# Optimization experiments

Hardware: AMD Instinct MI355X
Metric: run time of the kernel (lower is better)

The kernel has to match this reference:

```python
import jax, jax.numpy as jnp
import numpy as np
from jax.ops import segment_sum

N, E, F, H, G, T = 50000, 800000, 128, 256, 512, 4


def setup_inputs() -> dict:
    key = jax.random.key(0)
    ks = jax.random.split(key, 12)
    x = jax.random.normal(ks[0], (N, F), jnp.float32)
    edge_index = jax.random.randint(ks[1], (2, E), 0, N)
    batch = jnp.sort(jax.random.randint(ks[2], (N,), 0, G))
    num_atoms = jax.random.normal(ks[3], (G, 1), jnp.float32)
    def lin(k, fan_in, fan_out):
        s = 1.0 / np.sqrt(fan_in)
        return jax.random.uniform(k, (fan_in, fan_out), jnp.float32, -s, s)
    W1 = lin(ks[4], F, H); b1 = jnp.zeros((H,), jnp.float32)
    W2 = lin(ks[5], H, H); b2 = jnp.zeros((H,), jnp.float32)
    W3 = lin(ks[6], H + 1, 32); b3 = jnp.zeros((32,), jnp.float32)
    W4 = lin(ks[7], 32, T); b4 = jnp.zeros((T,), jnp.float32)
    return {"x": x, "edge_index": edge_index, "batch": batch, "num_atoms": num_atoms,
            "W1": W1, "b1": b1, "W2": W2, "b2": b2, "W3": W3, "b3": b3, "W4": W4, "b4": b4}


def _gcn_norm(edge_index, num_nodes):
    # PyG GCNConv default: add self-loops, symmetric D^-1/2 A D^-1/2 normalization
    loop = jnp.arange(num_nodes, dtype=edge_index.dtype)
    src = jnp.concatenate([edge_index[0], loop])
    dst = jnp.concatenate([edge_index[1], loop])
    deg = segment_sum(jnp.ones_like(dst, jnp.float32), dst, num_segments=num_nodes)
    dinv = jnp.where(deg > 0, jax.lax.rsqrt(jnp.maximum(deg, 1e-12)), 0.0)
    norm = dinv[src] * dinv[dst]  # [E+N]
    return src, dst, norm


def _gcn_conv(x, W, b, src, dst, norm, num_nodes):
    h = x @ W  # [N, out]
    agg = segment_sum(h[src] * norm[:, None], dst, num_segments=num_nodes)
    return agg + b


def reference(x, edge_index, batch, num_atoms, W1, b1, W2, b2, W3, b3, W4, b4):
    n = x.shape[0]
    src, dst, norm = _gcn_norm(edge_index, n)
    h = jax.nn.relu(_gcn_conv(x, W1, b1, src, dst, norm, n))   # dropout = identity (eval)
    h = jax.nn.relu(_gcn_conv(h, W2, b2, src, dst, norm, n))
    # global mean pool over graphs
    sums = segment_sum(h, batch, num_segments=G)               # [G, H]
    cnt = segment_sum(jnp.ones((n,), jnp.float32), batch, num_segments=G)
    pooled = sums / jnp.maximum(cnt, 1.0)[:, None]
    z = jnp.concatenate([pooled, num_atoms], axis=1)           # [G, H+1]
    z = jax.nn.relu(z @ W3 + b3)
    return z @ W4 + b4                                         # [G, T]
```

## Files before the change

### kernel.cpp

```cpp
#include <hip/hip_runtime.h>
#include <hip/hip_bf16.h>
#include <hip/hip_fp8.h>


#define NN 50000
#define EE 800000
#define FDIM 128
#define HDIM 256
#define GG 512
#define SCAN_NB ((NN + 255) / 256)

typedef __attribute__((ext_vector_type(8))) short short8;
typedef __attribute__((ext_vector_type(4))) float floatx4;
typedef __attribute__((ext_vector_type(2))) float floatx2;

__device__ __forceinline__ unsigned short f2bf(float f) {
    unsigned u = __float_as_uint(f);
    return (unsigned short)((u + 0x7FFF + ((u >> 16) & 1)) >> 16);
}
__device__ __forceinline__ float bflo(unsigned v) { return __uint_as_float(v << 16); }
__device__ __forceinline__ float bfhi(unsigned v) { return __uint_as_float(v & 0xFFFF0000u); }

__device__ __forceinline__ unsigned char enc8(float v) {
#if defined(__has_builtin) && __has_builtin(__builtin_amdgcn_cvt_pk_fp8_f32)
    return (unsigned char)(__builtin_amdgcn_cvt_pk_fp8_f32(v, v, 0, false) & 0xFF);
#else
    __hip_fp8_e4m3 q(v);
    return (unsigned char)q.__x;
#endif
}
__device__ __forceinline__ void dec4(int d, float* f) {
#if defined(__has_builtin) && __has_builtin(__builtin_amdgcn_cvt_pk_f32_fp8)
    floatx2 lo = __builtin_amdgcn_cvt_pk_f32_fp8(d, false);
    floatx2 hi = __builtin_amdgcn_cvt_pk_f32_fp8(d, true);
    f[0] = lo.x; f[1] = lo.y; f[2] = hi.x; f[3] = hi.y;
#else
    unsigned u = (unsigned)d;
    #pragma unroll
    for (int i = 0; i < 4; ++i) {
        __hip_fp8_e4m3 t; t.__x = (__hip_fp8_storage_t)((u >> (8 * i)) & 0xFF);
        f[i] = (float)t;
    }
#endif
}

__device__ __forceinline__ void gload16(const void* g, void* l) {
    __builtin_amdgcn_global_load_lds((const __attribute__((address_space(1))) void*)g,
                                     (__attribute__((address_space(3))) void*)l, 16, 0, 0);
}


__global__ void hist_kernel(const int* __restrict__ dst, int* __restrict__ deg,
                            int* __restrict__ epos, int e) {
    int i = blockIdx.x * blockDim.x + threadIdx.x;
    int stride = gridDim.x * blockDim.x;
    for (; i < e; i += stride) epos[i] = atomicAdd(&deg[dst[i]], 1);
}

__global__ __launch_bounds__(256) void scan_part(const int* __restrict__ deg,
                                                 int* __restrict__ row_off,
                                                 int* __restrict__ blk_sums,
                                                 float* __restrict__ dinv, int n) {
    __shared__ int s[256];
    int tid = threadIdx.x;
    int i = blockIdx.x * 256 + tid;
    int v = (i < n) ? deg[i] : 0;
    if (i < n) dinv[i] = rsqrtf((float)v + 1.0f);
    s[tid] = v;
    __syncthreads();
    #pragma unroll
    for (int off = 1; off < 256; off <<= 1) {
        int t = (tid >= off) ? s[tid - off] : 0;
        __syncthreads();
        s[tid] += t;
        __syncthreads();
    }
    if (i < n) row_off[i] = s[tid] - v;
    if (tid == 255) blk_sums[blockIdx.x] = s[255];
}

__global__ __launch_bounds__(256) void scan_sums(int* __restrict__ blk_sums, int nb) {
    __shared__ int s[256];
    int tid = threadIdx.x;
    int v = (tid < nb) ? blk_sums[tid] : 0;
    s[tid] = v;
    __syncthreads();
    #pragma unroll
    for (int off = 1; off < 256; off <<= 1) {
        int t = (tid >= off) ? s[tid - off] : 0;
        __syncthreads();
        s[tid] += t;
        __syncthreads();
    }
    if (tid < nb) blk_sums[tid] = s[tid] - v;
}

__global__ __launch_bounds__(256) void scan_add(int* __restrict__ row_off,
                                                const int* __restrict__ blk_sums,
                                                int n, int e) {
    int i = blockIdx.x * 256 + threadIdx.x;
    if (i < n) row_off[i] += blk_sums[blockIdx.x];
    if (i == 0) row_off[n] = e;
}

__global__ void scatter_kernel(const int* __restrict__ src, const int* __restrict__ dst,
                               const int* __restrict__ row_off, const int* __restrict__ epos,
                               const float* __restrict__ dinv,
                               int2* __restrict__ csr, int e) {
    int i = blockIdx.x * blockDim.x + threadIdx.x;
    int stride = gridDim.x * blockDim.x;
    for (; i < e; i += stride) {
        int s = src[i], d = dst[i];
        int pos = row_off[d] + epos[i];
        csr[pos] = make_int2(s, __float_as_int(dinv[s] * dinv[d]));
    }
}

#define XCHUNKS (NN * FDIM / 4)
#define CAST_TOTAL (XCHUNKS + FDIM * HDIM + HDIM * HDIM + NN / 4 + GG * HDIM / 4)
__global__ __launch_bounds__(256) void cast_all(const float* __restrict__ x,
                                                unsigned short* __restrict__ x_bf,
                                                const float* __restrict__ W1,
                                                unsigned short* __restrict__ W1t,
                                                const float* __restrict__ W2,
                                                unsigned short* __restrict__ W2t,
                                                int* __restrict__ deg,
                                                float* __restrict__ pool) {
    int idx = blockIdx.x * 256 + threadIdx.x;
    if (idx < XCHUNKS) {
        int i = idx * 4;
        float4 v = *(const float4*)&x[i];
        ushort4 o;
        o.x = f2bf(v.x); o.y = f2bf(v.y); o.z = f2bf(v.z); o.w = f2bf(v.w);
        *(ushort4*)&x_bf[i] = o;
        return;
    }
    int r = idx - XCHUNKS;
    if (r < FDIM * HDIM) {
        int nn = r / FDIM, k = r - nn * FDIM;
        W1t[r] = f2bf(W1[(size_t)k * HDIM + nn]);
        return;
    }
    r -= FDIM * HDIM;
    if (r < HDIM * HDIM) {
        int nn = r / HDIM, k = r - nn * HDIM;
        W2t[r] = f2bf(W2[(size_t)k * HDIM + nn]);
        return;
    }
    r -= HDIM * HDIM;
    if (r < NN / 4) {
        int4 z = {0, 0, 0, 0};
        *(int4*)&deg[r * 4] = z;
        return;
    }
    r -= NN / 4;
    if (r < GG * HDIM / 4) {
        float4 z = {0.f, 0.f, 0.f, 0.f};
        *(float4*)&pool[r * 4] = z;
    }
}


#define FMA8(v, wgt) do { unsigned _u; \
    _u = (unsigned)(v).x; acc0 = fmaf(bflo(_u), (wgt), acc0); acc1 = fmaf(bfhi(_u), (wgt), acc1); \
    _u = (unsigned)(v).y; acc2 = fmaf(bflo(_u), (wgt), acc2); acc3 = fmaf(bfhi(_u), (wgt), acc3); \
    _u = (unsigned)(v).z; acc4 = fmaf(bflo(_u), (wgt), acc4); acc5 = fmaf(bfhi(_u), (wgt), acc5); \
    _u = (unsigned)(v).w; acc6 = fmaf(bflo(_u), (wgt), acc6); acc7 = fmaf(bfhi(_u), (wgt), acc7); } while (0)

__device__ __forceinline__ void fma16(const int4& g, float wgt, float* acc) {
    float f[16];
    dec4(g.x, f); dec4(g.y, f + 4); dec4(g.z, f + 8); dec4(g.w, f + 12);
    #pragma unroll
    for (int i = 0; i < 16; ++i) acc[i] = fmaf(f[i], wgt, acc[i]);
}

__global__ __launch_bounds__(256) void gcn_agg256_fp8(const unsigned char* __restrict__ in,
                                                      const int* __restrict__ row_off,
                                                      const int2* __restrict__ csr,
                                                      const float* __restrict__ dinv,
                                                      unsigned short* __restrict__ out, int n) {
    int wave = threadIdx.x >> 6;
    int lane = threadIdx.x & 63;
    int node = blockIdx.x * 4 + wave;
    if (node >= n) return;
    int sub = lane >> 4;
    int fl  = lane & 15;
    float di = dinv[node];
    float w0 = (sub == 0) ? di * di : 0.f;

    float acc[16];
    {
        int4 sv = *(const int4*)&in[(size_t)node * 256 + fl * 16];
        float f[16];
        dec4(sv.x, f); dec4(sv.y, f + 4); dec4(sv.z, f + 8); dec4(sv.w, f + 12);
        #pragma unroll
        for (int i = 0; i < 16; ++i) acc[i] = f[i] * w0;
    }

    int beg = __builtin_amdgcn_readfirstlane(row_off[node]);
    int end = __builtin_amdgcn_readfirstlane(row_off[node + 1]);
    int cnt = end - beg;
    if (cnt > 0) {
        int nIter = (cnt + 7) >> 3;
        int base = beg;
        int last = end - 1;
        int i0 = base + sub, i1 = base + 4 + sub;
        int2 c0 = csr[i0 < end ? i0 : last];
        int2 c1 = csr[i1 < end ? i1 : last];
        for (int it = 0; it < nIter; ++it) {
            int4 g0 = *(const int4*)&in[(size_t)c0.x * 256 + fl * 16];
            int4 g1 = *(const int4*)&in[(size_t)c1.x * 256 + fl * 16];
            float we0 = (base + sub < end) ? __int_as_float(c0.y) : 0.f;
            float we1 = (base + 4 + sub < end) ? __int_as_float(c1.y) : 0.f;
            int nb = base + 8;
            int j0 = nb + sub, j1 = nb + 4 + sub;
            int2 n0 = csr[j0 < end ? j0 : last];
            int2 n1 = csr[j1 < end ? j1 : last];
            fma16(g0, we0, acc); fma16(g1, we1, acc);
            c0 = n0; c1 = n1; base = nb;
        }
    }
    #pragma unroll
    for (int i = 0; i < 16; ++i) {
        acc[i] += __shfl_xor(acc[i], 16);
        acc[i] += __shfl_xor(acc[i], 32);
    }
    if (sub == 0) {
        int4 o0, o1;
        o0.x = (int)((unsigned)f2bf(acc[0])  | ((unsigned)f2bf(acc[1])  << 16));
        o0.y = (int)((unsigned)f2bf(acc[2])  | ((unsigned)f2bf(acc[3])  << 16));
        o0.z = (int)((unsigned)f2bf(acc[4])  | ((unsigned)f2bf(acc[5])  << 16));
        o0.w = (int)((unsigned)f2bf(acc[6])  | ((unsigned)f2bf(acc[7])  << 16));
        o1.x = (int)((unsigned)f2bf(acc[8])  | ((unsigned)f2bf(acc[9])  << 16));
        o1.y = (int)((unsigned)f2bf(acc[10]) | ((unsigned)f2bf(acc[11]) << 16));
        o1.z = (int)((unsigned)f2bf(acc[12]) | ((unsigned)f2bf(acc[13]) << 16));
        o1.w = (int)((unsigned)f2bf(acc[14]) | ((unsigned)f2bf(acc[15]) << 16));
        *(int4*)&out[(size_t)node * 256 + fl * 16] = o0;
        *(int4*)&out[(size_t)node * 256 + fl * 16 + 8] = o1;
    }
}

__global__ __launch_bounds__(256) void gcn_agg128_bf16(const unsigned short* __restrict__ in,
                                                       const int* __restrict__ row_off,
                                                       const int2* __restrict__ csr,
                                                       const float* __restrict__ dinv,
                                                       unsigned short* __restrict__ out, int n) {
    int wave = threadIdx.x >> 6;
    int lane = threadIdx.x & 63;
    int node = blockIdx.x * 4 + wave;
    if (node >= n) return;
    int sub = lane >> 4;
    int fl  = lane & 15;
    float di = dinv[node];
    float w0 = (sub == 0) ? di * di : 0.f;

    float acc0, acc1, acc2, acc3, acc4, acc5, acc6, acc7;
    {
        int4 sv = *(const int4*)&in[(size_t)node * 128 + fl * 8];
        unsigned _u;
        _u = (unsigned)sv.x; acc0 = bflo(_u) * w0; acc1 = bfhi(_u) * w0;
        _u = (unsigned)sv.y; acc2 = bflo(_u) * w0; acc3 = bfhi(_u) * w0;
        _u = (unsigned)sv.z; acc4 = bflo(_u) * w0; acc5 = bfhi(_u) * w0;
        _u = (unsigned)sv.w; acc6 = bflo(_u) * w0; acc7 = bfhi(_u) * w0;
    }

    int beg = __builtin_amdgcn_readfirstlane(row_off[node]);
    int end = __builtin_amdgcn_readfirstlane(row_off[node + 1]);
    int cnt = end - beg;
    if (cnt > 0) {
        int nIter = (cnt + 7) >> 3;
        int base = beg;
        int last = end - 1;
        int i0 = base + sub, i1 = base + 4 + sub;
        int2 c0 = csr[i0 < end ? i0 : last];
        int2 c1 = csr[i1 < end ? i1 : last];
        for (int it = 0; it < nIter; ++it) {
            int4 g0 = *(const int4*)&in[(size_t)c0.x * 128 + fl * 8];
            int4 g1 = *(const int4*)&in[(size_t)c1.x * 128 + fl * 8];
            float we0 = (base + sub < end) ? __int_as_float(c0.y) : 0.f;
            float we1 = (base + 4 + sub < end) ? __int_as_float(c1.y) : 0.f;
            int nb = base + 8;
            int j0 = nb + sub, j1 = nb + 4 + sub;
            int2 n0 = csr[j0 < end ? j0 : last];
            int2 n1 = csr[j1 < end ? j1 : last];
            FMA8(g0, we0); FMA8(g1, we1);
            c0 = n0; c1 = n1; base = nb;
        }
    }
    acc0 += __shfl_xor(acc0, 16); acc1 += __shfl_xor(acc1, 16);
    acc2 += __shfl_xor(acc2, 16); acc3 += __shfl_xor(acc3, 16);
    acc4 += __shfl_xor(acc4, 16); acc5 += __shfl_xor(acc5, 16);
    acc6 += __shfl_xor(acc6, 16); acc7 += __shfl_xor(acc7, 16);
    acc0 += __shfl_xor(acc0, 32); acc1 += __shfl_xor(acc1, 32);
    acc2 += __shfl_xor(acc2, 32); acc3 += __shfl_xor(acc3, 32);
    acc4 += __shfl_xor(acc4, 32); acc5 += __shfl_xor(acc5, 32);
    acc6 += __shfl_xor(acc6, 32); acc7 += __shfl_xor(acc7, 32);
    if (sub == 0) {
        int4 o;
        o.x = (int)((unsigned)f2bf(acc0) | ((unsigned)f2bf(acc1) << 16));
        o.y = (int)((unsigned)f2bf(acc2) | ((unsigned)f2bf(acc3) << 16));
        o.z = (int)((unsigned)f2bf(acc4) | ((unsigned)f2bf(acc5) << 16));
        o.w = (int)((unsigned)f2bf(acc6) | ((unsigned)f2bf(acc7) << 16));
        *(int4*)&out[(size_t)node * 128 + fl * 8] = o;
    }
}


__global__ __launch_bounds__(512, 2) void gemm1_mfma_bias_relu(
        const unsigned short* __restrict__ A,
        const unsigned short* __restrict__ Bt,
        const float* __restrict__ bias,
        unsigned char* __restrict__ C, int M) {
    constexpr int K = FDIM, Nc = HDIM, LDT = 32;
    __shared__ unsigned short As[128 * LDT];
    __shared__ unsigned short Bs[256 * LDT];
    int tid = threadIdx.x;
    int lane = tid & 63, wave = tid >> 6;
    int wm = (wave >> 2) * 64, wn = (wave & 3) * 64;
    int bm = blockIdx.x * 128;
    int l15 = lane & 15, quad = lane >> 4;

    floatx4 zero = {0.f, 0.f, 0.f, 0.f};
    floatx4 acc[4][4];
    #pragma unroll
    for (int s = 0; s < 4; ++s)
        #pragma unroll
        for (int t = 0; t < 4; ++t) acc[s][t] = zero;

    for (int k0 = 0; k0 < K; k0 += 32) {
        {
            int c = tid;
            gload16(&A[(size_t)(bm + (c >> 2)) * K + k0 + (c & 3) * 8], &As[wave * 512]);
        }
        {
            int c = tid;
            gload16(&Bt[(size_t)(c >> 2) * K + k0 + (c & 3) * 8], &Bs[wave * 512]);
            int c2 = tid + 512;
            gload16(&Bt[(size_t)(c2 >> 2) * K + k0 + (c2 & 3) * 8], &Bs[4096 + wave * 512]);
        }
        __syncthreads();
        short8 af[4], bf[4];
        #pragma unroll
        for (int s = 0; s < 4; ++s)
            af[s] = *(const short8*)&As[(wm + s * 16 + l15) * LDT + quad * 8];
        #pragma unroll
        for (int t = 0; t < 4; ++t)
            bf[t] = *(const short8*)&Bs[(wn + t * 16 + l15) * LDT + quad * 8];
        #pragma unroll
        for (int s = 0; s < 4; ++s)
            #pragma unroll
            for (int t = 0; t < 4; ++t)
                acc[s][t] = __builtin_amdgcn_mfma_f32_16x16x32_bf16(af[s], bf[t], acc[s][t], 0, 0, 0);
        __syncthreads();
    }
    #pragma unroll
    for (int s = 0; s < 4; ++s) {
        int row0 = bm + wm + s * 16 + quad * 4;
        #pragma unroll
        for (int t = 0; t < 4; ++t) {
            int col = wn + t * 16 + l15;
            float bb = bias[col];
            #pragma unroll
            for (int r = 0; r < 4; ++r) {
                int row = row0 + r;
                if (row < M)
                    C[(size_t)row * Nc + col] = enc8(fmaxf(acc[s][t][r] + bb, 0.f));
            }
        }
    }
}

__global__ __launch_bounds__(512, 2) void gemm2_pool(
        const unsigned short* __restrict__ A,
        const unsigned short* __restrict__ Bt,
        const float* __restrict__ bias,
        const int* __restrict__ batch,
        float* __restrict__ pool, int M) {
    constexpr int K = HDIM, Nc = HDIM, LDT = 32;
    __shared__ unsigned short As[128 * LDT];
    __shared__ unsigned short Bs[256 * LDT];
    int tid = threadIdx.x;
    int lane = tid & 63, wave = tid >> 6;
    int wm = (wave >> 2) * 64, wn = (wave & 3) * 64;
    int bm = blockIdx.x * 128;
    int l15 = lane & 15, quad = lane >> 4;

    floatx4 zero = {0.f, 0.f, 0.f, 0.f};
    floatx4 acc[4][4];
    #pragma unroll
    for (int s = 0; s < 4; ++s)
        #pragma unroll
        for (int t = 0; t < 4; ++t) acc[s][t] = zero;

    for (int k0 = 0; k0 < K; k0 += 32) {
        {
            int c = tid;
            gload16(&A[(size_t)(bm + (c >> 2)) * K + k0 + (c & 3) * 8], &As[wave * 512]);
        }
        {
            int c = tid;
            gload16(&Bt[(size_t)(c >> 2) * K + k0 + (c & 3) * 8], &Bs[wave * 512]);
            int c2 = tid + 512;
            gload16(&Bt[(size_t)(c2 >> 2) * K + k0 + (c2 & 3) * 8], &Bs[4096 + wave * 512]);
        }
        __syncthreads();
        short8 af[4], bf[4];
        #pragma unroll
        for (int s = 0; s < 4; ++s)
            af[s] = *(const short8*)&As[(wm + s * 16 + l15) * LDT + quad * 8];
        #pragma unroll
        for (int t = 0; t < 4; ++t)
            bf[t] = *(const short8*)&Bs[(wn + t * 16 + l15) * LDT + quad * 8];
        #pragma unroll
        for (int s = 0; s < 4; ++s)
            #pragma unroll
            for (int t = 0; t < 4; ++t)
                acc[s][t] = __builtin_amdgcn_mfma_f32_16x16x32_bf16(af[s], bf[t], acc[s][t], 0, 0, 0);
        __syncthreads();
    }
    #pragma unroll
    for (int s = 0; s < 4; ++s) {
        int row0 = bm + wm + s * 16 + quad * 4;
        if (row0 >= M) continue;
        bool full = (row0 + 3 < M);
        int gA = batch[row0];
        int gB = full ? batch[row0 + 3] : gA;
        bool same = full && (gA == gB);
        #pragma unroll
        for (int t = 0; t < 4; ++t) {
            int col = wn + t * 16 + l15;
            float bb = bias[col];
            if (same) {
                float v = fmaxf(acc[s][t][0] + bb, 0.f) + fmaxf(acc[s][t][1] + bb, 0.f)
                        + fmaxf(acc[s][t][2] + bb, 0.f) + fmaxf(acc[s][t][3] + bb, 0.f);
                atomicAdd(&pool[(size_t)gA * Nc + col], v);
            } else {
                #pragma unroll
                for (int r = 0; r < 4; ++r) {
                    int row = row0 + r;
                    if (row < M) {
                        float v = fmaxf(acc[s][t][r] + bb, 0.f);
                        atomicAdd(&pool[(size_t)batch[row] * Nc + col], v);
                    }
                }
            }
        }
    }
}


__device__ __forceinline__ int lower_bound_i(const int* __restrict__ a, int n, int v) {
    int lo = 0, hi = n;
    while (lo < hi) {
        int mid = (lo + hi) >> 1;
        if (a[mid] < v) lo = mid + 1; else hi = mid;
    }
    return lo;
}

__global__ __launch_bounds__(256) void head_kernel(const float* __restrict__ pool,
                                                   const int* __restrict__ batch,
                                                   const float* __restrict__ num_atoms,
                                                   const float* __restrict__ W3, const float* __restrict__ b3,
                                                   const float* __restrict__ W4, const float* __restrict__ b4,
                                                   float* __restrict__ out, int n) {
    int g = blockIdx.x;
    int tid = threadIdx.x;
    __shared__ int s_lo, s_hi;
    if (tid == 0) {
        s_lo = lower_bound_i(batch, n, g);
        s_hi = lower_bound_i(batch, n, g + 1);
    }
    __syncthreads();
    float cnt = (float)(s_hi - s_lo);

    __shared__ float zin[HDIM + 1];
    __shared__ float z[32];
    zin[tid] = pool[(size_t)g * HDIM + tid] / fmaxf(cnt, 1.0f);
    if (tid == 0) zin[HDIM] = num_atoms[g];
    __syncthreads();
    if (tid < 32) {
        float a = b3[tid];
        for (int k = 0; k < HDIM + 1; ++k) a = fmaf(zin[k], W3[k * 32 + tid], a);
        z[tid] = fmaxf(a, 0.f);
    }
    __syncthreads();
    if (tid < 4) {
        float a = b4[tid];
        #pragma unroll
        for (int k = 0; k < 32; ++k) a = fmaf(z[k], W4[k * 4 + tid], a);
        out[g * 4 + tid] = a;
    }
}


extern "C" void kernel_launch(void* const* d_in, const int* in_sizes, int n_in,
                              void* d_out, int out_size, void* d_ws, size_t ws_size,
                              hipStream_t stream) {
    const float* x         = (const float*)d_in[0];
    const int*   edge_idx  = (const int*)d_in[1];
    const int*   batch     = (const int*)d_in[2];
    const float* num_atoms = (const float*)d_in[3];
    const float* W1 = (const float*)d_in[4];
    const float* b1 = (const float*)d_in[5];
    const float* W2 = (const float*)d_in[6];
    const float* b2 = (const float*)d_in[7];
    const float* W3 = (const float*)d_in[8];
    const float* b3 = (const float*)d_in[9];
    const float* W4 = (const float*)d_in[10];
    const float* b4 = (const float*)d_in[11];
    float* out = (float*)d_out;

    const int n = NN, e = EE;
    const int* e_src = edge_idx;
    const int* e_dst = edge_idx + e;

    char* ws = (char*)d_ws;
    size_t off = 0;
    auto carve = [&](size_t bytes) -> void* {
        void* p = ws + off;
        off = (off + bytes + 255) & ~(size_t)255;
        return p;
    };
    int*   deg_i    = (int*)carve((size_t)n * 4);
    int*   row_off  = (int*)carve((size_t)(n + 1) * 4);
    int*   blk_sums = (int*)carve((size_t)256 * 4);
    float* dinv     = (float*)carve((size_t)n * 4);
    int*   epos     = (int*)carve((size_t)e * 4);
    unsigned short* W1t = (unsigned short*)carve((size_t)FDIM * HDIM * 2);
    unsigned short* W2t = (unsigned short*)carve((size_t)HDIM * HDIM * 2);
    int2*  csr      = (int2*)carve((size_t)e * 8);
    unsigned short* P = (unsigned short*)carve((size_t)n * HDIM * 2);
    unsigned char*  Q = (unsigned char*)carve((size_t)n * HDIM);
    float* pool     = (float*)carve((size_t)GG * HDIM * 4);
    unsigned short* x_bf = P;
    unsigned short* a0b  = P + (size_t)n * FDIM;
    unsigned short* a1b  = P;
    unsigned char*  h1f8 = Q;
    (void)ws_size; (void)n_in; (void)in_sizes; (void)out_size;

    cast_all<<<(CAST_TOTAL + 255) / 256, 256, 0, stream>>>(
        x, x_bf, W1, W1t, W2, W2t, deg_i, pool);
    hist_kernel<<<1024, 256, 0, stream>>>(e_dst, deg_i, epos, e);
    scan_part<<<SCAN_NB, 256, 0, stream>>>(deg_i, row_off, blk_sums, dinv, n);
    scan_sums<<<1, 256, 0, stream>>>(blk_sums, SCAN_NB);
    scan_add<<<SCAN_NB, 256, 0, stream>>>(row_off, blk_sums, n, e);
    scatter_kernel<<<1024, 256, 0, stream>>>(e_src, e_dst, row_off, epos, dinv, csr, e);

    int gemm_grid = (n + 127) / 128;
    gcn_agg128_bf16<<<(n + 3) / 4, 256, 0, stream>>>(x_bf, row_off, csr, dinv, a0b, n);
    gemm1_mfma_bias_relu<<<gemm_grid, 512, 0, stream>>>(a0b, W1t, b1, h1f8, n);
    gcn_agg256_fp8<<<(n + 3) / 4, 256, 0, stream>>>(h1f8, row_off, csr, dinv, a1b, n);
    gemm2_pool<<<gemm_grid, 512, 0, stream>>>(a1b, W2t, b2, batch, pool, n);
    head_kernel<<<GG, 256, 0, stream>>>(pool, batch, num_atoms, W3, b3, W4, b4, out, n);
}
```

Measured before the change: 297.0 us.

## Double-buffer GEMM LDS tiles and split output columns across a 2D grid

```diff
diff --git a/kernel.cpp b/kernel.cpp
--- a/kernel.cpp
+++ b/kernel.cpp
@@ -312,53 +312,54 @@
         const float* __restrict__ bias,
         unsigned char* __restrict__ C, int M) {
     constexpr int K = FDIM, Nc = HDIM, LDT = 32;
-    __shared__ unsigned short As[128 * LDT];
-    __shared__ unsigned short Bs[256 * LDT];
+    __shared__ unsigned short As[2][128 * LDT];
+    __shared__ unsigned short Bs[2][128 * LDT];
     int tid = threadIdx.x;
     int lane = tid & 63, wave = tid >> 6;
-    int wm = (wave >> 2) * 64, wn = (wave & 3) * 64;
+    int wm = (wave >> 2) * 64;
+    int wn2 = (wave & 3) * 32;
     int bm = blockIdx.x * 128;
+    int bn = blockIdx.y * 128;
     int l15 = lane & 15, quad = lane >> 4;
+    int srow = tid >> 2, sq = (tid & 3) * 8;
 
     floatx4 zero = {0.f, 0.f, 0.f, 0.f};
-    floatx4 acc[4][4];
+    floatx4 acc[4][2];
     #pragma unroll
     for (int s = 0; s < 4; ++s)
         #pragma unroll
-        for (int t = 0; t < 4; ++t) acc[s][t] = zero;
-
+        for (int t = 0; t < 2; ++t) acc[s][t] = zero;
+
+    gload16(&A[(size_t)(bm + srow) * K + sq], &As[0][wave * 512]);
+    gload16(&Bt[(size_t)(bn + srow) * K + sq], &Bs[0][wave * 512]);
+    __syncthreads();
+    int cur = 0;
     for (int k0 = 0; k0 < K; k0 += 32) {
-        {
-            int c = tid;
-            gload16(&A[(size_t)(bm + (c >> 2)) * K + k0 + (c & 3) * 8], &As[wave * 512]);
+        if (k0 + 32 < K) {
+            gload16(&A[(size_t)(bm + srow) * K + k0 + 32 + sq], &As[cur ^ 1][wave * 512]);
+            gload16(&Bt[(size_t)(bn + srow) * K + k0 + 32 + sq], &Bs[cur ^ 1][wave * 512]);
         }
-        {
-            int c = tid;
-            gload16(&Bt[(size_t)(c >> 2) * K + k0 + (c & 3) * 8], &Bs[wave * 512]);
-            int c2 = tid + 512;
-            gload16(&Bt[(size_t)(c2 >> 2) * K + k0 + (c2 & 3) * 8], &Bs[4096 + wave * 512]);
-        }
-        __syncthreads();
-        short8 af[4], bf[4];
+        short8 af[4], bf[2];
         #pragma unroll
         for (int s = 0; s < 4; ++s)
-            af[s] = *(const short8*)&As[(wm + s * 16 + l15) * LDT + quad * 8];
-        #pragma unroll
-        for (int t = 0; t < 4; ++t)
-            bf[t] = *(const short8*)&Bs[(wn + t * 16 + l15) * LDT + quad * 8];
+            af[s] = *(const short8*)&As[cur][(wm + s * 16 + l15) * LDT + quad * 8];
+        #pragma unroll
+        for (int t = 0; t < 2; ++t)
+            bf[t] = *(const short8*)&Bs[cur][(wn2 + t * 16 + l15) * LDT + quad * 8];
         #pragma unroll
         for (int s = 0; s < 4; ++s)
             #pragma unroll
-            for (int t = 0; t < 4; ++t)
+            for (int t = 0; t < 2; ++t)
                 acc[s][t] = __builtin_amdgcn_mfma_f32_16x16x32_bf16(af[s], bf[t], acc[s][t], 0, 0, 0);
         __syncthreads();
+        cur ^= 1;
     }
     #pragma unroll
     for (int s = 0; s < 4; ++s) {
         int row0 = bm + wm + s * 16 + quad * 4;
         #pragma unroll
-        for (int t = 0; t < 4; ++t) {
-            int col = wn + t * 16 + l15;
+        for (int t = 0; t < 2; ++t) {
+            int col = bn + wn2 + t * 16 + l15;
             float bb = bias[col];
             #pragma unroll
             for (int r = 0; r < 4; ++r) {
@@ -377,46 +378,47 @@
         const int* __restrict__ batch,
         float* __restrict__ pool, int M) {
     constexpr int K = HDIM, Nc = HDIM, LDT = 32;
-    __shared__ unsigned short As[128 * LDT];
-    __shared__ unsigned short Bs[256 * LDT];
+    __shared__ unsigned short As[2][128 * LDT];
+    __shared__ unsigned short Bs[2][128 * LDT];
     int tid = threadIdx.x;
     int lane = tid & 63, wave = tid >> 6;
-    int wm = (wave >> 2) * 64, wn = (wave & 3) * 64;
+    int wm = (wave >> 2) * 64;
+    int wn2 = (wave & 3) * 32;
     int bm = blockIdx.x * 128;
+    int bn = blockIdx.y * 128;
     int l15 = lane & 15, quad = lane >> 4;
+    int srow = tid >> 2, sq = (tid & 3) * 8;
 
     floatx4 zero = {0.f, 0.f, 0.f, 0.f};
-    floatx4 acc[4][4];
+    floatx4 acc[4][2];
     #pragma unroll
     for (int s = 0; s < 4; ++s)
         #pragma unroll
-        for (int t = 0; t < 4; ++t) acc[s][t] = zero;
-
+        for (int t = 0; t < 2; ++t) acc[s][t] = zero;
+
+    gload16(&A[(size_t)(bm + srow) * K + sq], &As[0][wave * 512]);
+    gload16(&Bt[(size_t)(bn + srow) * K + sq], &Bs[0][wave * 512]);
+    __syncthreads();
+    int cur = 0;
     for (int k0 = 0; k0 < K; k0 += 32) {
-        {
-            int c = tid;
-            gload16(&A[(size_t)(bm + (c >> 2)) * K + k0 + (c & 3) * 8], &As[wave * 512]);
+        if (k0 + 32 < K) {
+            gload16(&A[(size_t)(bm + srow) * K + k0 + 32 + sq], &As[cur ^ 1][wave * 512]);
+            gload16(&Bt[(size_t)(bn + srow) * K + k0 + 32 + sq], &Bs[cur ^ 1][wave * 512]);
         }
-        {
-            int c = tid;
-            gload16(&Bt[(size_t)(c >> 2) * K + k0 + (c & 3) * 8], &Bs[wave * 512]);
-            int c2 = tid + 512;
-            gload16(&Bt[(size_t)(c2 >> 2) * K + k0 + (c2 & 3) * 8], &Bs[4096 + wave * 512]);
-        }
-        __syncthreads();
-        short8 af[4], bf[4];
+        short8 af[4], bf[2];
         #pragma unroll
         for (int s = 0; s < 4; ++s)
-            af[s] = *(const short8*)&As[(wm + s * 16 + l15) * LDT + quad * 8];
-        #pragma unroll
-        for (int t = 0; t < 4; ++t)
-            bf[t] = *(const short8*)&Bs[(wn + t * 16 + l15) * LDT + quad * 8];
+            af[s] = *(const short8*)&As[cur][(wm + s * 16 + l15) * LDT + quad * 8];
+        #pragma unroll
+        for (int t = 0; t < 2; ++t)
+            bf[t] = *(const short8*)&Bs[cur][(wn2 + t * 16 + l15) * LDT + quad * 8];
         #pragma unroll
         for (int s = 0; s < 4; ++s)
             #pragma unroll
-            for (int t = 0; t < 4; ++t)
+            for (int t = 0; t < 2; ++t)
                 acc[s][t] = __builtin_amdgcn_mfma_f32_16x16x32_bf16(af[s], bf[t], acc[s][t], 0, 0, 0);
         __syncthreads();
+        cur ^= 1;
     }
     #pragma unroll
     for (int s = 0; s < 4; ++s) {
@@ -427,8 +429,8 @@
         int gB = full ? batch[row0 + 3] : gA;
         bool same = full && (gA == gB);
         #pragma unroll
-        for (int t = 0; t < 4; ++t) {
-            int col = wn + t * 16 + l15;
+        for (int t = 0; t < 2; ++t) {
+            int col = bn + wn2 + t * 16 + l15;
             float bb = bias[col];
             if (same) {
                 float v = fmaxf(acc[s][t][0] + bb, 0.f) + fmaxf(acc[s][t][1] + bb, 0.f)
@@ -547,7 +549,7 @@
     scan_add<<<SCAN_NB, 256, 0, stream>>>(row_off, blk_sums, n, e);
     scatter_kernel<<<1024, 256, 0, stream>>>(e_src, e_dst, row_off, epos, dinv, csr, e);
 
-    int gemm_grid = (n + 127) / 128;
+    dim3 gemm_grid((n + 127) / 128, 2);
     gcn_agg128_bf16<<<(n + 3) / 4, 256, 0, stream>>>(x_bf, row_off, csr, dinv, a0b, n);
     gemm1_mfma_bias_relu<<<gemm_grid, 512, 0, stream>>>(a0b, W1t, b1, h1f8, n);
     gcn_agg256_fp8<<<(n + 3) / 4, 256, 0, stream>>>(h1f8, row_off, csr, dinv, a1b, n);
```

Measured after the change: 300.3 us. About the same (+1.1%).
